# Optimization experiments

Hardware: AMD Instinct MI355X
Metric: run time of the kernel (lower is better)

Reference implementation:

```python
import jax, jax.numpy as jnp
import numpy as np

N = 50000
E = 800000
IN_DIM = 256
HID = 128
OUT = 64


def setup_inputs() -> dict:
    key = jax.random.key(0)
    ks = jax.random.split(key, 12)
    inp = {}
    inp["x"] = jax.random.normal(ks[0], (N, IN_DIM), dtype=jnp.float32)
    inp["edge_index"] = jax.random.randint(ks[1], (2, E), 0, N, dtype=jnp.int64)
    s0 = 1.0 / np.sqrt(IN_DIM)
    inp["W0"] = jax.random.uniform(ks[2], (IN_DIM, HID), jnp.float32, -s0, s0)
    inp["b0"] = jax.random.uniform(ks[3], (HID,), jnp.float32, -s0, s0)
    sa = 1.0 / np.sqrt(2 * HID)
    inp["att_w1"] = jax.random.uniform(ks[4], (2 * HID, 1), jnp.float32, -sa, sa)
    inp["att_b1"] = jax.random.uniform(ks[5], (1,), jnp.float32, -sa, sa)
    inp["eps1"] = jnp.float32(0.1)
    inp["att_w2"] = jax.random.uniform(ks[6], (2 * HID, 1), jnp.float32, -sa, sa)
    inp["att_b2"] = jax.random.uniform(ks[7], (1,), jnp.float32, -sa, sa)
    inp["eps2"] = jnp.float32(0.1)
    sc = 1.0 / np.sqrt(HID)
    inp["Wc"] = jax.random.uniform(ks[8], (HID, OUT), jnp.float32, -sc, sc)
    inp["bc"] = jax.random.uniform(ks[9], (OUT,), jnp.float32, -sc, sc)
    return inp


def _fagcn_layer(x, row, col, att_w, att_b, eps):
    # x: [N, H]; row/col: [E]
    x_i = x[row]                       # [E, H] source (gathered)
    x_j = x[col]                       # [E, H] destination
    # cat([x_i, x_j]) @ att_w == x_i @ att_w[:H] + x_j @ att_w[H:]
    H = x.shape[1]
    score = x_i @ att_w[:H] + x_j @ att_w[H:] + att_b  # [E, 1]
    alpha = jnp.tanh(score)            # [E, 1]
    messages = alpha * x_i             # [E, H]
    agg = jax.ops.segment_sum(messages, col, num_segments=x.shape[0])  # [N, H]
    return eps * x + (1.0 - eps) * agg


def reference(x, edge_index, W0, b0, att_w1, att_b1, eps1, att_w2, att_b2, eps2, Wc, bc):
    row, col = edge_index[0], edge_index[1]
    h = jax.nn.relu(x @ W0 + b0)       # initial linear + relu (dropout=eval identity)
    h = jax.nn.relu(_fagcn_layer(h, row, col, att_w1, att_b1, eps1))
    h = jax.nn.relu(_fagcn_layer(h, row, col, att_w2, att_b2, eps2))
    return h @ Wc + bc                 # [N, OUT]
```

## Files before the change

kernel.cpp:

```cpp
#include <hip/hip_runtime.h>

#define N_NODES 50000
#define E_EDGES 800000
#define IN_DIM 256
#define HID 128
#define OUT_DIM 64
#define SLOT 64

#define LR 64
#define NBUILD ((E_EDGES / 8 + 255) / 256)
#define NLIN ((N_NODES + LR - 1) / LR)

typedef unsigned short u16;
typedef __attribute__((ext_vector_type(8))) short short8;
typedef __attribute__((ext_vector_type(4))) float floatx4;

__device__ __forceinline__ u16 f2bf(float f) {
    unsigned u = __float_as_uint(f);
    unsigned r = (u + 0x7FFFu + ((u >> 16) & 1u)) >> 16;
    return (u16)r;
}
__device__ __forceinline__ void bf8_unpack(uint4 v, float* f) {
    f[0] = __uint_as_float(v.x << 16); f[1] = __uint_as_float(v.x & 0xffff0000u);
    f[2] = __uint_as_float(v.y << 16); f[3] = __uint_as_float(v.y & 0xffff0000u);
    f[4] = __uint_as_float(v.z << 16); f[5] = __uint_as_float(v.z & 0xffff0000u);
    f[6] = __uint_as_float(v.w << 16); f[7] = __uint_as_float(v.w & 0xffff0000u);
}
__device__ __forceinline__ uint4 bf8_pack(const float* f) {
    uint4 o;
    o.x = f2bf(f[0]) | ((unsigned)f2bf(f[1]) << 16);
    o.y = f2bf(f[2]) | ((unsigned)f2bf(f[3]) << 16);
    o.z = f2bf(f[4]) | ((unsigned)f2bf(f[5]) << 16);
    o.w = f2bf(f[6]) | ((unsigned)f2bf(f[7]) << 16);
    return o;
}

__global__ __launch_bounds__(256) void k_pre(const float* __restrict__ W0,
                                             const float* __restrict__ Wc,
                                             u16* __restrict__ W0T,
                                             u16* __restrict__ Wct,
                                             int* __restrict__ cnt) {
    const int gid = blockIdx.x * 256 + threadIdx.x;
    if (gid < N_NODES / 4) ((int4*)cnt)[gid] = (int4){0, 0, 0, 0};
    if (gid < IN_DIM * HID) {
        const int n = gid >> 8, k = gid & (IN_DIM - 1);
        W0T[gid] = f2bf(W0[k * HID + n]);
    }
    if (gid < HID * OUT_DIM) {
        const int o = gid >> 7, k = gid & (HID - 1);
        Wct[gid] = f2bf(Wc[k * OUT_DIM + o]);
    }
}

__global__ __launch_bounds__(256) void k_front(
    const float* __restrict__ x, const u16* __restrict__ W0T,
    const float* __restrict__ b0, const float* __restrict__ aw1,
    u16* __restrict__ h, float* __restrict__ sa, float* __restrict__ sb,
    const int* __restrict__ ei, int* __restrict__ cnt,
    u16* __restrict__ srcidx) {
    if (blockIdx.x < NBUILD) {
        const int gid = blockIdx.x * 256 + threadIdx.x;
        if (gid >= E_EDGES / 8) return;
        const int4 w0 = ((const int4*)ei)[2 * gid];
        const int4 w1 = ((const int4*)ei)[2 * gid + 1];
        const int4 c0 = ((const int4*)(ei + E_EDGES))[2 * gid];
        const int4 c1 = ((const int4*)(ei + E_EDGES))[2 * gid + 1];
        const int p0 = atomicAdd(&cnt[c0.x], 1);
        const int p1 = atomicAdd(&cnt[c0.y], 1);
        const int p2 = atomicAdd(&cnt[c0.z], 1);
        const int p3 = atomicAdd(&cnt[c0.w], 1);
        const int p4 = atomicAdd(&cnt[c1.x], 1);
        const int p5 = atomicAdd(&cnt[c1.y], 1);
        const int p6 = atomicAdd(&cnt[c1.z], 1);
        const int p7 = atomicAdd(&cnt[c1.w], 1);
        if (p0 < SLOT) srcidx[(c0.x << 6) + p0] = (u16)w0.x;
        if (p1 < SLOT) srcidx[(c0.y << 6) + p1] = (u16)w0.y;
        if (p2 < SLOT) srcidx[(c0.z << 6) + p2] = (u16)w0.z;
        if (p3 < SLOT) srcidx[(c0.w << 6) + p3] = (u16)w0.w;
        if (p4 < SLOT) srcidx[(c1.x << 6) + p4] = (u16)w1.x;
        if (p5 < SLOT) srcidx[(c1.y << 6) + p5] = (u16)w1.y;
        if (p6 < SLOT) srcidx[(c1.z << 6) + p6] = (u16)w1.z;
        if (p7 < SLOT) srcidx[(c1.w << 6) + p7] = (u16)w1.w;
        return;
    }

    const int t = threadIdx.x;
    const int lane = t & 63;
    const int w = t >> 6;
    const int sub = lane & 15;
    const int quad = lane >> 4;
    const int row0 = (blockIdx.x - NBUILD) * LR;

    int gr_a = row0 + w * 16 + sub;
    if (gr_a > N_NODES - 1) gr_a = N_NODES - 1;
    const float* xrow = x + (size_t)gr_a * IN_DIM + quad * 8;
    const u16* wbase = W0T + (size_t)sub * IN_DIM + quad * 8;

    floatx4 acc[8];
    #pragma unroll
    for (int i = 0; i < 8; ++i) acc[i] = (floatx4){0.f, 0.f, 0.f, 0.f};

    #pragma unroll
    for (int ks = 0; ks < IN_DIM; ks += 32) {
        const float4 f0 = *(const float4*)(xrow + ks);
        const float4 f1 = *(const float4*)(xrow + ks + 4);
        union { uint4 u; short8 s; } a;
        a.u.x = f2bf(f0.x) | ((unsigned)f2bf(f0.y) << 16);
        a.u.y = f2bf(f0.z) | ((unsigned)f2bf(f0.w) << 16);
        a.u.z = f2bf(f1.x) | ((unsigned)f2bf(f1.y) << 16);
        a.u.w = f2bf(f1.z) | ((unsigned)f2bf(f1.w) << 16);
        #pragma unroll
        for (int ct = 0; ct < 8; ++ct) {
            const short8 bb = *(const short8*)(wbase + ct * 16 * IN_DIM + ks);
            acc[ct] = __builtin_amdgcn_mfma_f32_16x16x32_bf16(a.s, bb, acc[ct], 0, 0, 0);
        }
    }

    float bias[8], w1c[8], w2c[8];
    #pragma unroll
    for (int ct = 0; ct < 8; ++ct) {
        const int col = ct * 16 + sub;
        bias[ct] = b0[col];
        w1c[ct] = aw1[col];
        w2c[ct] = aw1[HID + col];
    }
    #pragma unroll
    for (int reg = 0; reg < 4; ++reg) {
        const int gr = row0 + w * 16 + quad * 4 + reg;
        const bool ok = gr < N_NODES;
        float ps = 0.f, pd = 0.f;
        #pragma unroll
        for (int ct = 0; ct < 8; ++ct) {
            const float val = fmaxf(acc[ct][reg] + bias[ct], 0.f);
            if (ok) h[(size_t)gr * HID + ct * 16 + sub] = f2bf(val);
            ps += val * w1c[ct];
            pd += val * w2c[ct];
        }
        #pragma unroll
        for (int off = 1; off < 16; off <<= 1) {
            ps += __shfl_xor(ps, off);
            pd += __shfl_xor(pd, off);
        }
        if (sub == 0 && ok) { sa[gr] = ps; sb[gr] = pd; }
    }
}

__global__ __launch_bounds__(256) void k_agg(const u16* __restrict__ hin,
                                             const float* __restrict__ sa,
                                             const float* __restrict__ sb,
                                             const float* __restrict__ attb,
                                             const float* __restrict__ epsp,
                                             const int* __restrict__ cnt,
                                             const u16* __restrict__ srcidx,
                                             u16* __restrict__ hout,
                                             const float* __restrict__ attw_next,
                                             float* __restrict__ sa_next,
                                             float* __restrict__ sb_next) {
    const int qid = threadIdx.x >> 4;
    const int sub = threadIdx.x & 15;
    const int n = blockIdx.x * 16 + qid;
    if (n >= N_NODES) return;
    const float b = attb[0];
    const float sbn = sb[n];
    const int beg = n << 6;
    int deg = cnt[n];
    if (deg > SLOT) deg = SLOT;
    const int end = beg + deg;
    float acc[8];
    #pragma unroll
    for (int j = 0; j < 8; ++j) acc[j] = 0.f;

    int e = beg;
    uint4 svn;
    if (e + 8 <= end) svn = *(const uint4*)(srcidx + e);
    for (; e + 8 <= end; e += 8) {
        const uint4 sv = svn;
        if (e + 16 <= end) svn = *(const uint4*)(srcidx + e + 8);
        int s[8];
        s[0] = (int)(sv.x & 0xffffu); s[1] = (int)(sv.x >> 16);
        s[2] = (int)(sv.y & 0xffffu); s[3] = (int)(sv.y >> 16);
        s[4] = (int)(sv.z & 0xffffu); s[5] = (int)(sv.z >> 16);
        s[6] = (int)(sv.w & 0xffffu); s[7] = (int)(sv.w >> 16);
        uint4 v[8];
        #pragma unroll
        for (int i = 0; i < 8; ++i)
            v[i] = *(const uint4*)(hin + (size_t)s[i] * HID + sub * 8);
        const float tt = tanhf(sa[s[sub & 7]] + sbn + b);
        float al[8];
        #pragma unroll
        for (int i = 0; i < 8; ++i) al[i] = __shfl(tt, i, 16);
        #pragma unroll
        for (int i = 0; i < 8; ++i) {
            float f[8];
            bf8_unpack(v[i], f);
            #pragma unroll
            for (int j = 0; j < 8; ++j) acc[j] += al[i] * f[j];
        }
    }
    const int rem = end - e;
    if (rem > 0) {
        const int sfirst = (int)srcidx[e];
        int s[8];
        #pragma unroll
        for (int i = 0; i < 8; ++i) s[i] = (i < rem) ? (int)srcidx[e + i] : sfirst;
        const float tt = ((sub & 7) < rem) ? tanhf(sa[s[sub & 7]] + sbn + b) : 0.f;
        float al[8];
        #pragma unroll
        for (int i = 0; i < 8; ++i) al[i] = __shfl(tt, i, 16);
        #pragma unroll
        for (int i = 0; i < 8; ++i) {
            if (i < rem) {
                const uint4 v = *(const uint4*)(hin + (size_t)s[i] * HID + sub * 8);
                float f[8];
                bf8_unpack(v, f);
                #pragma unroll
                for (int j = 0; j < 8; ++j) acc[j] += al[i] * f[j];
            }
        }
    }

    const float eps = epsp[0];
    const float om = 1.f - eps;
    const uint4 sv = *(const uint4*)(hin + (size_t)n * HID + sub * 8);
    float self[8], hv[8];
    bf8_unpack(sv, self);
    #pragma unroll
    for (int j = 0; j < 8; ++j)
        hv[j] = fmaxf(eps * self[j] + om * acc[j], 0.f);
    *(uint4*)(hout + (size_t)n * HID + sub * 8) = bf8_pack(hv);

    if (attw_next != nullptr) {
        float psum = 0.f, dsum = 0.f;
        #pragma unroll
        for (int j = 0; j < 8; ++j) {
            psum += hv[j] * attw_next[sub * 8 + j];
            dsum += hv[j] * attw_next[HID + sub * 8 + j];
        }
        #pragma unroll
        for (int off = 1; off < 16; off <<= 1) {
            psum += __shfl_xor(psum, off);
            dsum += __shfl_xor(dsum, off);
        }
        if (sub == 0) { sa_next[n] = psum; sb_next[n] = dsum; }
    }
}

__global__ __launch_bounds__(256) void k_out_mfma(const u16* __restrict__ h,
                                                  const u16* __restrict__ Wct,
                                                  const float* __restrict__ bc,
                                                  float* __restrict__ out) {
    const int t = threadIdx.x;
    const int lane = t & 63;
    const int w = t >> 6;
    const int sub = lane & 15;
    const int quad = lane >> 4;
    const int row0 = blockIdx.x * LR;

    int gr_a = row0 + w * 16 + sub;
    if (gr_a > N_NODES - 1) gr_a = N_NODES - 1;
    const u16* hrow = h + (size_t)gr_a * HID + quad * 8;
    const u16* wbase = Wct + (size_t)sub * HID + quad * 8;

    floatx4 acc[4];
    #pragma unroll
    for (int j = 0; j < 4; ++j) acc[j] = (floatx4){0.f, 0.f, 0.f, 0.f};

    #pragma unroll
    for (int ks = 0; ks < HID; ks += 32) {
        const short8 a = *(const short8*)(hrow + ks);
        #pragma unroll
        for (int ct = 0; ct < 4; ++ct) {
            const short8 bb = *(const short8*)(wbase + ct * 16 * HID + ks);
            acc[ct] = __builtin_amdgcn_mfma_f32_16x16x32_bf16(a, bb, acc[ct], 0, 0, 0);
        }
    }

    #pragma unroll
    for (int ct = 0; ct < 4; ++ct) {
        const float bias = bc[ct * 16 + sub];
        #pragma unroll
        for (int reg = 0; reg < 4; ++reg) {
            const int gr = row0 + w * 16 + quad * 4 + reg;
            if (gr < N_NODES)
                out[(size_t)gr * OUT_DIM + ct * 16 + sub] = acc[ct][reg] + bias;
        }
    }
}

extern "C" void kernel_launch(void* const* d_in, const int* in_sizes, int n_in,
                              void* d_out, int out_size, void* d_ws, size_t ws_size,
                              hipStream_t stream) {
    const float* x   = (const float*)d_in[0];
    const int*   ei  = (const int*)d_in[1];
    const float* W0  = (const float*)d_in[2];
    const float* b0  = (const float*)d_in[3];
    const float* aw1 = (const float*)d_in[4];
    const float* ab1 = (const float*)d_in[5];
    const float* e1  = (const float*)d_in[6];
    const float* aw2 = (const float*)d_in[7];
    const float* ab2 = (const float*)d_in[8];
    const float* e2  = (const float*)d_in[9];
    const float* Wc  = (const float*)d_in[10];
    const float* bc  = (const float*)d_in[11];
    float* out = (float*)d_out;

    u16* hA  = (u16*)d_ws;
    u16* hB  = hA + (size_t)N_NODES * HID;
    u16* W0T = hB + (size_t)N_NODES * HID;
    u16* Wct = W0T + IN_DIM * HID;
    float* sa1 = (float*)(Wct + HID * OUT_DIM);
    float* sb1 = sa1 + N_NODES;
    float* sa2 = sb1 + N_NODES;
    float* sb2 = sa2 + N_NODES;
    int* cnt    = (int*)(sb2 + N_NODES);
    u16* srcidx = (u16*)(cnt + N_NODES);

    k_pre<<<128, 256, 0, stream>>>(W0, Wc, W0T, Wct, cnt);
    k_front<<<NBUILD + NLIN, 256, 0, stream>>>(x, W0T, b0, aw1, hA, sa1, sb1,
                                               ei, cnt, srcidx);
    k_agg<<<(N_NODES + 15) / 16, 256, 0, stream>>>(hA, sa1, sb1, ab1, e1, cnt, srcidx,
                                                   hB, aw2, sa2, sb2);
    k_agg<<<(N_NODES + 15) / 16, 256, 0, stream>>>(hB, sa2, sb2, ab2, e2, cnt, srcidx,
                                                   hA, nullptr, nullptr, nullptr);
    k_out_mfma<<<NLIN, 256, 0, stream>>>(hA, Wct, bc, out);
}
```

Before: 255.4 us.

## Stage x tile in LDS for linear layer; widen gather loop to 16 edges

The front linear kernel now loads the 64-row x tile with coalesced float4 reads, converts it to bf16 into padded shared memory, and feeds the MFMA A operand from LDS, where each lane previously read strided rows straight from global memory. The aggregation kernel processes 16 neighbours per iteration instead of 8, issuing 16 independent row gathers for more memory-level parallelism. It also hoists the self-row load to the start. The costs are extra LDS and a barrier in the front kernel and higher register pressure in the aggregation kernel. The remainder path now reads 16 indices unconditionally, which can run past a node's filled slots but stays inside its 64-slot segment.

```diff
diff --git a/kernel.cpp b/kernel.cpp
--- a/kernel.cpp
+++ b/kernel.cpp
@@ -8,6 +8,7 @@
 #define SLOT 64
 
 #define LR 64
+#define AP 264
 #define NBUILD ((E_EDGES / 8 + 255) / 256)
 #define NLIN ((N_NODES + LR - 1) / LR)
 
@@ -58,6 +59,7 @@
     u16* __restrict__ h, float* __restrict__ sa, float* __restrict__ sb,
     const int* __restrict__ ei, int* __restrict__ cnt,
     u16* __restrict__ srcidx) {
+    __shared__ u16 As[LR][AP];
     if (blockIdx.x < NBUILD) {
         const int gid = blockIdx.x * 256 + threadIdx.x;
         if (gid >= E_EDGES / 8) return;
@@ -91,28 +93,35 @@
     const int quad = lane >> 4;
     const int row0 = (blockIdx.x - NBUILD) * LR;
 
-    int gr_a = row0 + w * 16 + sub;
-    if (gr_a > N_NODES - 1) gr_a = N_NODES - 1;
-    const float* xrow = x + (size_t)gr_a * IN_DIM + quad * 8;
+    {
+        const int rsub = t >> 6;
+        const int c4 = (t & 63) * 4;
+        #pragma unroll
+        for (int j = 0; j < 16; ++j) {
+            const int r = 4 * j + rsub;
+            int gr = row0 + r;
+            if (gr > N_NODES - 1) gr = N_NODES - 1;
+            const float4 f = *(const float4*)(x + (size_t)gr * IN_DIM + c4);
+            uint2 p;
+            p.x = f2bf(f.x) | ((unsigned)f2bf(f.y) << 16);
+            p.y = f2bf(f.z) | ((unsigned)f2bf(f.w) << 16);
+            *(uint2*)&As[r][c4] = p;
+        }
+    }
+    __syncthreads();
+
+    floatx4 acc[8];
+    #pragma unroll
+    for (int i = 0; i < 8; ++i) acc[i] = (floatx4){0.f, 0.f, 0.f, 0.f};
+
     const u16* wbase = W0T + (size_t)sub * IN_DIM + quad * 8;
-
-    floatx4 acc[8];
-    #pragma unroll
-    for (int i = 0; i < 8; ++i) acc[i] = (floatx4){0.f, 0.f, 0.f, 0.f};
-
     #pragma unroll
     for (int ks = 0; ks < IN_DIM; ks += 32) {
-        const float4 f0 = *(const float4*)(xrow + ks);
-        const float4 f1 = *(const float4*)(xrow + ks + 4);
-        union { uint4 u; short8 s; } a;
-        a.u.x = f2bf(f0.x) | ((unsigned)f2bf(f0.y) << 16);
-        a.u.y = f2bf(f0.z) | ((unsigned)f2bf(f0.w) << 16);
-        a.u.z = f2bf(f1.x) | ((unsigned)f2bf(f1.y) << 16);
-        a.u.w = f2bf(f1.z) | ((unsigned)f2bf(f1.w) << 16);
+        const short8 a = *(const short8*)&As[w * 16 + sub][ks + quad * 8];
         #pragma unroll
         for (int ct = 0; ct < 8; ++ct) {
             const short8 bb = *(const short8*)(wbase + ct * 16 * IN_DIM + ks);
-            acc[ct] = __builtin_amdgcn_mfma_f32_16x16x32_bf16(a.s, bb, acc[ct], 0, 0, 0);
+            acc[ct] = __builtin_amdgcn_mfma_f32_16x16x32_bf16(a, bb, acc[ct], 0, 0, 0);
         }
     }
 
@@ -166,31 +175,34 @@
     int deg = cnt[n];
     if (deg > SLOT) deg = SLOT;
     const int end = beg + deg;
+    const uint4 svself = *(const uint4*)(hin + (size_t)n * HID + sub * 8);
     float acc[8];
     #pragma unroll
     for (int j = 0; j < 8; ++j) acc[j] = 0.f;
 
     int e = beg;
-    uint4 svn;
-    if (e + 8 <= end) svn = *(const uint4*)(srcidx + e);
-    for (; e + 8 <= end; e += 8) {
-        const uint4 sv = svn;
-        if (e + 16 <= end) svn = *(const uint4*)(srcidx + e + 8);
-        int s[8];
-        s[0] = (int)(sv.x & 0xffffu); s[1] = (int)(sv.x >> 16);
-        s[2] = (int)(sv.y & 0xffffu); s[3] = (int)(sv.y >> 16);
-        s[4] = (int)(sv.z & 0xffffu); s[5] = (int)(sv.z >> 16);
-        s[6] = (int)(sv.w & 0xffffu); s[7] = (int)(sv.w >> 16);
-        uint4 v[8];
-        #pragma unroll
-        for (int i = 0; i < 8; ++i)
+    for (; e + 16 <= end; e += 16) {
+        const uint4 i0 = *(const uint4*)(srcidx + e);
+        const uint4 i1 = *(const uint4*)(srcidx + e + 8);
+        int s[16];
+        s[0]  = (int)(i0.x & 0xffffu); s[1]  = (int)(i0.x >> 16);
+        s[2]  = (int)(i0.y & 0xffffu); s[3]  = (int)(i0.y >> 16);
+        s[4]  = (int)(i0.z & 0xffffu); s[5]  = (int)(i0.z >> 16);
+        s[6]  = (int)(i0.w & 0xffffu); s[7]  = (int)(i0.w >> 16);
+        s[8]  = (int)(i1.x & 0xffffu); s[9]  = (int)(i1.x >> 16);
+        s[10] = (int)(i1.y & 0xffffu); s[11] = (int)(i1.y >> 16);
+        s[12] = (int)(i1.z & 0xffffu); s[13] = (int)(i1.z >> 16);
+        s[14] = (int)(i1.w & 0xffffu); s[15] = (int)(i1.w >> 16);
+        uint4 v[16];
+        #pragma unroll
+        for (int i = 0; i < 16; ++i)
             v[i] = *(const uint4*)(hin + (size_t)s[i] * HID + sub * 8);
-        const float tt = tanhf(sa[s[sub & 7]] + sbn + b);
-        float al[8];
-        #pragma unroll
-        for (int i = 0; i < 8; ++i) al[i] = __shfl(tt, i, 16);
-        #pragma unroll
-        for (int i = 0; i < 8; ++i) {
+        const float tt = tanhf(sa[s[sub]] + sbn + b);
+        float al[16];
+        #pragma unroll
+        for (int i = 0; i < 16; ++i) al[i] = __shfl(tt, i, 16);
+        #pragma unroll
+        for (int i = 0; i < 16; ++i) {
             float f[8];
             bf8_unpack(v[i], f);
             #pragma unroll
@@ -199,16 +211,23 @@
     }
     const int rem = end - e;
     if (rem > 0) {
-        const int sfirst = (int)srcidx[e];
-        int s[8];
-        #pragma unroll
-        for (int i = 0; i < 8; ++i) s[i] = (i < rem) ? (int)srcidx[e + i] : sfirst;
-        const float tt = ((sub & 7) < rem) ? tanhf(sa[s[sub & 7]] + sbn + b) : 0.f;
-        float al[8];
-        #pragma unroll
-        for (int i = 0; i < 8; ++i) al[i] = __shfl(tt, i, 16);
-        #pragma unroll
-        for (int i = 0; i < 8; ++i) {
+        const uint4 i0 = *(const uint4*)(srcidx + e);
+        const uint4 i1 = *(const uint4*)(srcidx + e + 8);
+        int s[16];
+        s[0]  = (int)(i0.x & 0xffffu); s[1]  = (int)(i0.x >> 16);
+        s[2]  = (int)(i0.y & 0xffffu); s[3]  = (int)(i0.y >> 16);
+        s[4]  = (int)(i0.z & 0xffffu); s[5]  = (int)(i0.z >> 16);
+        s[6]  = (int)(i0.w & 0xffffu); s[7]  = (int)(i0.w >> 16);
+        s[8]  = (int)(i1.x & 0xffffu); s[9]  = (int)(i1.x >> 16);
+        s[10] = (int)(i1.y & 0xffffu); s[11] = (int)(i1.y >> 16);
+        s[12] = (int)(i1.z & 0xffffu); s[13] = (int)(i1.z >> 16);
+        s[14] = (int)(i1.w & 0xffffu); s[15] = (int)(i1.w >> 16);
+        const float tt = (sub < rem) ? tanhf(sa[s[sub]] + sbn + b) : 0.f;
+        float al[16];
+        #pragma unroll
+        for (int i = 0; i < 16; ++i) al[i] = __shfl(tt, i, 16);
+        #pragma unroll
+        for (int i = 0; i < 16; ++i) {
             if (i < rem) {
                 const uint4 v = *(const uint4*)(hin + (size_t)s[i] * HID + sub * 8);
                 float f[8];
@@ -221,9 +240,8 @@
 
     const float eps = epsp[0];
     const float om = 1.f - eps;
-    const uint4 sv = *(const uint4*)(hin + (size_t)n * HID + sub * 8);
     float self[8], hv[8];
-    bf8_unpack(sv, self);
+    bf8_unpack(svself, self);
     #pragma unroll
     for (int j = 0; j < 8; ++j)
         hv[j] = fmaxf(eps * self[j] + om * acc[j], 0.f);
```

Result: slower. 286.2 us (+12.1%).
